# Kernel tuning notes

Measured on AMD Instinct MI355X. Metric: run time of the kernel, lower is better.

The kernel has to match this reference:

```python
import jax, jax.numpy as jnp
import numpy as np

B, N, DIM = 4, 8192, 1024
HEADS, DIM_HEAD = 16, 64


def setup_inputs() -> dict:
    key = jax.random.key(0)
    ks = jax.random.split(key, 6)
    s = 1.0 / np.sqrt(DIM_HEAD)
    so = 1.0 / np.sqrt(HEADS * DIM_HEAD)
    return {
        "x": jax.random.normal(ks[0], (B, N, DIM), dtype=jnp.float32),
        "Wq": jax.random.uniform(ks[1], (DIM_HEAD, DIM_HEAD), jnp.float32, -s, s),
        "Wk": jax.random.uniform(ks[2], (DIM_HEAD, DIM_HEAD), jnp.float32, -s, s),
        "Wv": jax.random.uniform(ks[3], (DIM_HEAD, DIM_HEAD), jnp.float32, -s, s),
        "Wo": jax.random.uniform(ks[4], (DIM, HEADS * DIM_HEAD), jnp.float32, -so, so),
        "bo": jax.random.uniform(ks[5], (DIM,), jnp.float32, -so, so),
    }


def reference(x, Wq, Wk, Wv, Wo, bo):
    Bs, Ns, Cs = x.shape
    # [B, H, N, Dh]
    xh = x.reshape(Bs, Ns, HEADS, DIM_HEAD).transpose(0, 2, 1, 3)
    # torch Linear: y = x @ W.T
    q = jnp.einsum('bhnd,ed->bhne', xh, Wq)
    k = jnp.einsum('bhnd,ed->bhne', xh, Wk)
    v = jnp.einsum('bhnd,ed->bhne', xh, Wv)
    # k^T v: [B, H, Dh, Dh], normalized by N (dropout is identity, p=0)
    dots = jnp.einsum('bhnd,bhne->bhde', k, v) / float(Ns)
    res = jnp.einsum('bhnd,bhde->bhne', q, dots)
    # b h n d -> b n (h d)
    res = res.transpose(0, 2, 1, 3).reshape(Bs, Ns, HEADS * DIM_HEAD)
    return res @ Wo.T + bo
```

## Files before the change

kernel.cpp:

```cpp
#include <hip/hip_runtime.h>

#define DIMC 1024
#define NSEQ 8192
#define DH 64

typedef __attribute__((ext_vector_type(8))) short short8;
typedef __attribute__((ext_vector_type(4))) float f32x4;

__device__ __forceinline__ short f2bf(float f) {
  union { float f; unsigned u; } v; v.f = f;
  unsigned r = v.u + 0x7FFFu + ((v.u >> 16) & 1u);
  return (short)(r >> 16);
}

__device__ __forceinline__ unsigned pack_bf2(float a, float b) {
  union { float f; unsigned u; } va, vb;
  va.f = a; vb.f = b;
  unsigned ua = va.u + 0x8000u;
  unsigned ub = vb.u + 0x8000u;
  return (ua >> 16) | (ub & 0xFFFF0000u);
}

__device__ __forceinline__ unsigned bfbits(float f) {
  union { float f; unsigned u; } v; v.f = f;
  return (v.u + 0x8000u) >> 16;
}
__device__ __forceinline__ float bf2f(unsigned hb) {
  union { unsigned u; float f; } v; v.u = hb << 16;
  return v.f;
}

__device__ __forceinline__ void gload_lds16(const void* g, void* l) {
  __builtin_amdgcn_global_load_lds(
      (const __attribute__((address_space(1))) void*)g,
      (__attribute__((address_space(3))) void*)l, 16, 0, 0);
}

__global__ __launch_bounds__(256) void gram2_kernel(const float* __restrict__ x,
                                                    float* __restrict__ Gpart,
                                                    short* __restrict__ xbf) {
  int chunk = blockIdx.x, bh = blockIdx.y;
  int b = bh >> 4, h = bh & 15;
  int t = threadIdx.x;
  int w = t >> 6, l = t & 63;
  int quad = l >> 4, ln = l & 15;

  __shared__ __align__(16) short XT[4][2][64 * 32];
  short* XH = &XT[w][0][0];
  short* XL = &XT[w][1][0];

  size_t rowbase = (size_t)b * NSEQ + (size_t)chunk * 1024 + w * 256;
  const float* xb = x + rowbase * DIMC + h * DH;
  short* xo = xbf + rowbase * DIMC + h * DH;

  f32x4 acc[4][4];
#pragma unroll
  for (int i = 0; i < 4; i++)
#pragma unroll
    for (int j = 0; j < 4; j++) acc[i][j] = (f32x4){0.f, 0.f, 0.f, 0.f};

  int woff[4][4];
#pragma unroll
  for (int q = 0; q < 4; q++) {
    int kk = 8 * q + 2 * quad;
    int kp = kk ^ ((ln & 3) << 3);
#pragma unroll
    for (int i = 0; i < 4; i++) {
      int d = ln * 4 + i;
      woff[q][i] = d * 32 + kp;
    }
  }
  int roff[4];
  {
    int k0 = (quad * 8) ^ ((ln >> 2) << 3);
#pragma unroll
    for (int i = 0; i < 4; i++) roff[i] = (i * 16 + ln) * 32 + k0;
  }

  float4 cur[4][2];
#pragma unroll
  for (int q = 0; q < 4; q++)
#pragma unroll
    for (int r = 0; r < 2; r++)
      cur[q][r] = *(const float4*)(xb + (size_t)(8 * q + 2 * quad + r) * DIMC + ln * 4);

  for (int ks = 0; ks < 8; ks++) {
    float4 nxt[4][2];
    if (ks < 7) {
      int nb = (ks + 1) * 32;
#pragma unroll
      for (int q = 0; q < 4; q++)
#pragma unroll
        for (int r = 0; r < 2; r++)
          nxt[q][r] = *(const float4*)(xb + (size_t)(nb + 8 * q + 2 * quad + r) * DIMC + ln * 4);
    }
#pragma unroll
    for (int q = 0; q < 4; q++) {
      unsigned h0[4], h1[4], l0[4], l1[4];
#pragma unroll
      for (int i = 0; i < 4; i++) {
        float a = cur[q][0][i], bb = cur[q][1][i];
        h0[i] = bfbits(a); l0[i] = bfbits(a - bf2f(h0[i]));
        h1[i] = bfbits(bb); l1[i] = bfbits(bb - bf2f(h1[i]));
      }
      int grow = ks * 32 + 8 * q + 2 * quad;
      uint2 p0 = {h0[0] | (h0[1] << 16), h0[2] | (h0[3] << 16)};
      uint2 p1 = {h1[0] | (h1[1] << 16), h1[2] | (h1[3] << 16)};
      *(uint2*)(xo + (size_t)grow * DIMC + ln * 4) = p0;
      *(uint2*)(xo + (size_t)(grow + 1) * DIMC + ln * 4) = p1;
#pragma unroll
      for (int i = 0; i < 4; i++) {
        *(unsigned*)&XH[woff[q][i]] = h0[i] | (h1[i] << 16);
        *(unsigned*)&XL[woff[q][i]] = l0[i] | (l1[i] << 16);
      }
    }
    short8 hf[4], lf[4];
#pragma unroll
    for (int i = 0; i < 4; i++) {
      hf[i] = *(const short8*)&XH[roff[i]];
      lf[i] = *(const short8*)&XL[roff[i]];
    }
#pragma unroll
    for (int i = 0; i < 4; i++)
#pragma unroll
      for (int j = 0; j < 4; j++) {
        acc[i][j] = __builtin_amdgcn_mfma_f32_16x16x32_bf16(hf[i], hf[j], acc[i][j], 0, 0, 0);
        acc[i][j] = __builtin_amdgcn_mfma_f32_16x16x32_bf16(hf[i], lf[j], acc[i][j], 0, 0, 0);
        acc[i][j] = __builtin_amdgcn_mfma_f32_16x16x32_bf16(lf[i], hf[j], acc[i][j], 0, 0, 0);
      }
#pragma unroll
    for (int q = 0; q < 4; q++)
#pragma unroll
      for (int r = 0; r < 2; r++) cur[q][r] = nxt[q][r];
  }

  float* gp = Gpart + (size_t)(chunk * 4 + w) * (64 * 4096) + (size_t)bh * 4096;
#pragma unroll
  for (int i = 0; i < 4; i++)
#pragma unroll
    for (int j = 0; j < 4; j++)
#pragma unroll
      for (int r = 0; r < 4; r++) {
        int d = i * 16 + quad * 4 + r, e = j * 16 + ln;
        gp[d * 64 + e] = acc[i][j][r];
      }
}

__global__ __launch_bounds__(64) void gram_kernel(const float* __restrict__ x,
                                                  float* __restrict__ Gpart,
                                                  short* __restrict__ xbf) {
  int chunk = blockIdx.x, bh = blockIdx.y;
  int b = bh >> 4, h = bh & 15;
  int t = threadIdx.x;
  __shared__ __align__(16) float rows[16 * 64];
  const float* xb = x + ((size_t)b * NSEQ) * DIMC + h * DH;
  short* xo = xbf ? xbf + ((size_t)b * NSEQ) * DIMC + h * DH : (short*)0;
  int d0 = (t >> 3) * 8, e0 = (t & 7) * 8;
  float acc[8][8] = {};
  float4 v[4];
#pragma unroll
  for (int i = 0; i < 4; i++) {
    int f4 = i * 64 + t;
    v[i] = *(const float4*)(xb + (size_t)(chunk * 256 + (f4 >> 4)) * DIMC + (f4 & 15) * 4);
  }
  for (int it = 0; it < 16; it++) {
    __syncthreads();
#pragma unroll
    for (int i = 0; i < 4; i++) ((float4*)rows)[i * 64 + t] = v[i];
    __syncthreads();
    if (xo) {
#pragma unroll
      for (int i = 0; i < 4; i++) {
        int f4 = i * 64 + t;
        int row = chunk * 256 + it * 16 + (f4 >> 4), col = (f4 & 15) * 4;
        uint2 pw = {pack_bf2(v[i].x, v[i].y), pack_bf2(v[i].z, v[i].w)};
        *(uint2*)(xo + (size_t)row * DIMC + col) = pw;
      }
    }
    if (it < 15) {
      int nbase = chunk * 256 + (it + 1) * 16;
#pragma unroll
      for (int i = 0; i < 4; i++) {
        int f4 = i * 64 + t;
        v[i] = *(const float4*)(xb + (size_t)(nbase + (f4 >> 4)) * DIMC + (f4 & 15) * 4);
      }
    }
#pragma unroll
    for (int r = 0; r < 16; r++) {
      float xd[8], xe[8];
      *(float4*)&xd[0] = *(const float4*)&rows[r * 64 + d0];
      *(float4*)&xd[4] = *(const float4*)&rows[r * 64 + d0 + 4];
      *(float4*)&xe[0] = *(const float4*)&rows[r * 64 + e0];
      *(float4*)&xe[4] = *(const float4*)&rows[r * 64 + e0 + 4];
#pragma unroll
      for (int i = 0; i < 8; i++)
#pragma unroll
        for (int j = 0; j < 8; j++) acc[i][j] = fmaf(xd[i], xe[j], acc[i][j]);
    }
  }
  float* gp = Gpart + (size_t)chunk * (64 * 4096) + (size_t)bh * 4096;
#pragma unroll
  for (int i = 0; i < 8; i++)
#pragma unroll
    for (int j = 0; j < 8; j++) gp[(d0 + i) * 64 + e0 + j] = acc[i][j];
}

__global__ void reduce_g(const float* __restrict__ Gpart, float* __restrict__ G) {
  int i = blockIdx.x * 256 + threadIdx.x;
  float s = 0.f;
#pragma unroll
  for (int p = 0; p < 32; p++) s += Gpart[(size_t)p * (64 * 4096) + i];
  G[i] = s;
}

__global__ __launch_bounds__(256) void combine_kernel(
    const float* __restrict__ G, const float* __restrict__ Wq,
    const float* __restrict__ Wk, const float* __restrict__ Wv,
    const float* __restrict__ Wo, short* __restrict__ WbigT) {
  int bh = blockIdx.x, qt = blockIdx.y;
  int b = bh >> 4, h = bh & 15;
  int t = threadIdx.x;
  __shared__ __align__(16) float sG[4096];
  __shared__ __align__(16) float sW[4096];
  __shared__ __align__(16) float sA[4096];
  __shared__ __align__(16) float sM[4096];

  for (int i = t; i < 4096; i += 256) sG[i] = G[(size_t)bh * 4096 + i];
  for (int i = t; i < 4096; i += 256) sW[i] = Wk[i];
  __syncthreads();

  int d0 = (t >> 4) * 4, e0 = (t & 15) * 4;
  {
    float a[4][4] = {};
    for (int fg = 0; fg < 16; fg++) {
      float wk[4][4], g4[4][4];
#pragma unroll
      for (int i = 0; i < 4; i++) *(float4*)wk[i] = *(const float4*)&sW[(d0 + i) * 64 + fg * 4];
#pragma unroll
      for (int ff = 0; ff < 4; ff++) *(float4*)g4[ff] = *(const float4*)&sG[(fg * 4 + ff) * 64 + e0];
#pragma unroll
      for (int i = 0; i < 4; i++)
#pragma unroll
        for (int ff = 0; ff < 4; ff++)
#pragma unroll
          for (int j = 0; j < 4; j++) a[i][j] = fmaf(wk[i][ff], g4[ff][j], a[i][j]);
    }
#pragma unroll
    for (int i = 0; i < 4; i++)
#pragma unroll
      for (int j = 0; j < 4; j++) sA[(d0 + i) * 64 + e0 + j] = a[i][j];
  }
  __syncthreads();
  for (int i = t; i < 4096; i += 256) sW[i] = Wv[i];
  __syncthreads();
  {
    float a[4][4] = {};
    for (int fgi = 0; fgi < 16; fgi++) {
      int fg = (fgi + (t & 15)) & 15;
      float t1[4][4], wv[4][4];
#pragma unroll
      for (int i = 0; i < 4; i++) *(float4*)t1[i] = *(const float4*)&sA[(d0 + i) * 64 + fg * 4];
#pragma unroll
      for (int j = 0; j < 4; j++) *(float4*)wv[j] = *(const float4*)&sW[(e0 + j) * 64 + fg * 4];
#pragma unroll
      for (int i = 0; i < 4; i++)
#pragma unroll
        for (int j = 0; j < 4; j++)
#pragma unroll
          for (int ff = 0; ff < 4; ff++) a[i][j] = fmaf(t1[i][ff], wv[j][ff], a[i][j]);
    }
    __syncthreads();
#pragma unroll
    for (int i = 0; i < 4; i++)
#pragma unroll
      for (int j = 0; j < 4; j++) sG[(d0 + i) * 64 + e0 + j] = a[i][j];
  }
  __syncthreads();
  for (int i = t; i < 4096; i += 256) sW[i] = Wq[i];
  __syncthreads();
  {
    float a[4][4] = {};
    for (int f = 0; f < 64; f++) {
      float wq[4], t2[4];
      *(float4*)wq = *(const float4*)&sW[f * 64 + d0];
      *(float4*)t2 = *(const float4*)&sG[f * 64 + e0];
#pragma unroll
      for (int i = 0; i < 4; i++)
#pragma unroll
        for (int j = 0; j < 4; j++) a[i][j] = fmaf(wq[i], t2[j], a[i][j]);
    }
#pragma unroll
    for (int i = 0; i < 4; i++)
#pragma unroll
      for (int j = 0; j < 4; j++) sM[(d0 + i) * 64 + e0 + j] = a[i][j] * (1.0f / 8192.0f);
  }
  __syncthreads();
  int dd0 = (t & 15) * 4, cl0 = (t >> 4) * 4;
  for (int cc = qt * 2; cc < qt * 2 + 2; cc++) {
    int c0 = cc * 64;
    for (int i = t; i < 4096; i += 256)
      sW[i] = Wo[(size_t)(c0 + (i >> 6)) * DIMC + h * DH + (i & 63)];
    __syncthreads();
    float a[4][4] = {};
    for (int egi = 0; egi < 16; egi++) {
      int eg = (egi + (t & 15)) & 15;
      float m4[4][4], wo4[4][4];
#pragma unroll
      for (int i = 0; i < 4; i++) *(float4*)m4[i] = *(const float4*)&sM[(dd0 + i) * 64 + eg * 4];
#pragma unroll
      for (int j = 0; j < 4; j++) *(float4*)wo4[j] = *(const float4*)&sW[(cl0 + j) * 64 + eg * 4];
#pragma unroll
      for (int i = 0; i < 4; i++)
#pragma unroll
        for (int j = 0; j < 4; j++)
#pragma unroll
          for (int ff = 0; ff < 4; ff++) a[i][j] = fmaf(m4[i][ff], wo4[j][ff], a[i][j]);
    }
#pragma unroll
    for (int j = 0; j < 4; j++) {
      uint2 pw = {pack_bf2(a[0][j], a[1][j]), pack_bf2(a[2][j], a[3][j])};
      *(uint2*)&WbigT[((size_t)b << 20) + (size_t)(c0 + cl0 + j) * DIMC + h * DH + dd0] = pw;
    }
    __syncthreads();
  }
}

__global__ __launch_bounds__(256, 3) void gemm_small(
    const float* __restrict__ x, const short* __restrict__ WbigT,
    const float* __restrict__ bo, float* __restrict__ out) {
  int bid = blockIdx.x;
  int xcd = bid & 7, r = bid >> 3;
  int g = r >> 5, q = r & 31;
  int m_blk = g * 32 + xcd * 4 + (q >> 3);
  int n_blk = q & 7;
  int b = m_blk >> 6;
  int row0 = m_blk * 128;
  int c0 = n_blk * 128;

  __shared__ __align__(16) short As[128 * 32];
  __shared__ __align__(16) short Bs[128 * 32];

  int t = threadIdx.x;
  int lane = t & 63, wave = t >> 6;
  int wm = wave >> 1, wn = wave & 1;
  int quad = lane >> 4, ln = lane & 15;

  f32x4 acc[4][4];
#pragma unroll
  for (int i = 0; i < 4; i++)
#pragma unroll
    for (int j = 0; j < 4; j++) acc[i][j] = (f32x4){0.f, 0.f, 0.f, 0.f};

  const short* Bbase = WbigT + ((size_t)b << 20);

  int e_base[2], crow_[2], lc_[2];
#pragma unroll
  for (int L = 0; L < 2; L++) {
    int e = (wave * 2 + L) * 512 + lane * 8;
    e_base[L] = e;
    int crow = e >> 5;
    crow_[L] = crow;
    lc_[L] = ((e >> 3) & 3) ^ ((crow >> 1) & 3);
  }

  for (int kt = 0; kt < 32; kt++) {
    int k0 = kt * 32;
    __syncthreads();
#pragma unroll
    for (int L = 0; L < 2; L++)
      gload_lds16(Bbase + (size_t)(c0 + crow_[L]) * DIMC + k0 + lc_[L] * 8, &Bs[e_base[L]]);
#pragma unroll
    for (int qq = 0; qq < 2; qq++) {
      int elem = qq * 2048 + wave * 512 + lane * 8;
      int m = elem >> 5, kk = elem & 31;
      const float* gp = x + (size_t)(row0 + m) * DIMC + k0 + kk;
      float4 v0 = *(const float4*)gp;
      float4 v1 = *(const float4*)(gp + 4);
      unsigned w0 = pack_bf2(v0.x, v0.y), w1 = pack_bf2(v0.z, v0.w);
      unsigned w2 = pack_bf2(v1.x, v1.y), w3 = pack_bf2(v1.z, v1.w);
      unsigned tmp[4] = {w0, w1, w2, w3};
      int pe = ((elem >> 3) & 3) ^ ((m >> 1) & 3);
      *(short8*)&As[m * 32 + pe * 8] = *(short8*)tmp;
    }
    __syncthreads();
    short8 afrag[4], bfrag[4];
#pragma unroll
    for (int i = 0; i < 4; i++) {
      int ar = wm * 64 + i * 16 + ln;
      afrag[i] = *(const short8*)&As[ar * 32 + (quad ^ ((ar >> 1) & 3)) * 8];
      int br = wn * 64 + i * 16 + ln;
      bfrag[i] = *(const short8*)&Bs[br * 32 + (quad ^ ((br >> 1) & 3)) * 8];
    }
#pragma unroll
    for (int i = 0; i < 4; i++)
#pragma unroll
      for (int j = 0; j < 4; j++)
        acc[i][j] = __builtin_amdgcn_mfma_f32_16x16x32_bf16(afrag[i], bfrag[j], acc[i][j], 0, 0, 0);
  }

  float bov[4];
#pragma unroll
  for (int j = 0; j < 4; j++) bov[j] = bo[c0 + wn * 64 + j * 16 + ln];
#pragma unroll
  for (int i = 0; i < 4; i++)
#pragma unroll
    for (int j = 0; j < 4; j++) {
      int col = c0 + wn * 64 + j * 16 + ln;
#pragma unroll
      for (int rr = 0; rr < 4; rr++) {
        int row = row0 + wm * 64 + i * 16 + quad * 4 + rr;
        out[(size_t)row * DIMC + col] = acc[i][j][rr] + bov[j];
      }
    }
}

__global__ __launch_bounds__(256, 3) void gemm_big(
    const short* __restrict__ xbf, const short* __restrict__ WbigT,
    const float* __restrict__ bo, float* __restrict__ out) {
  int bid = blockIdx.x;
  int xcd = bid & 7, r = bid >> 3;
  int g = r >> 5, q = r & 31;
  int m_blk = g * 32 + xcd * 4 + (q >> 3);
  int n_blk = q & 7;
  int b = m_blk >> 6;
  int row0 = m_blk * 128;
  int c0 = n_blk * 128;

  __shared__ __align__(16) short As[128 * 32];
  __shared__ __align__(16) short Bs[128 * 32];

  int t = threadIdx.x;
  int lane = t & 63, wave = t >> 6;
  int wm = wave >> 1, wn = wave & 1;
  int quad = lane >> 4, ln = lane & 15;

  f32x4 acc[4][4];
#pragma unroll
  for (int i = 0; i < 4; i++)
#pragma unroll
    for (int j = 0; j < 4; j++) acc[i][j] = (f32x4){0.f, 0.f, 0.f, 0.f};

  const short* Bbase = WbigT + ((size_t)b << 20);

  int e_base[2];
  const short* Asrc[2];
  const short* Bsrc[2];
#pragma unroll
  for (int L = 0; L < 2; L++) {
    int e = (wave * 2 + L) * 512 + lane * 8;
    e_base[L] = e;
    int row = e >> 5;
    int lc = ((e >> 3) & 3) ^ ((row >> 1) & 3);
    Asrc[L] = xbf + (size_t)(row0 + row) * DIMC + lc * 8;
    Bsrc[L] = Bbase + (size_t)(c0 + row) * DIMC + lc * 8;
  }

  for (int kt = 0; kt < 32; kt++) {
    int k0 = kt * 32;
    __syncthreads();
#pragma unroll
    for (int L = 0; L < 2; L++) gload_lds16(Asrc[L] + k0, &As[e_base[L]]);
#pragma unroll
    for (int L = 0; L < 2; L++) gload_lds16(Bsrc[L] + k0, &Bs[e_base[L]]);
    __syncthreads();
    short8 afrag[4], bfrag[4];
#pragma unroll
    for (int i = 0; i < 4; i++) {
      int ar = wm * 64 + i * 16 + ln;
      afrag[i] = *(const short8*)&As[ar * 32 + (quad ^ ((ar >> 1) & 3)) * 8];
      int br = wn * 64 + i * 16 + ln;
      bfrag[i] = *(const short8*)&Bs[br * 32 + (quad ^ ((br >> 1) & 3)) * 8];
    }
#pragma unroll
    for (int i = 0; i < 4; i++)
#pragma unroll
      for (int j = 0; j < 4; j++)
        acc[i][j] = __builtin_amdgcn_mfma_f32_16x16x32_bf16(afrag[i], bfrag[j], acc[i][j], 0, 0, 0);
  }

  float bov[4];
#pragma unroll
  for (int j = 0; j < 4; j++) bov[j] = bo[c0 + wn * 64 + j * 16 + ln];
#pragma unroll
  for (int i = 0; i < 4; i++)
#pragma unroll
    for (int j = 0; j < 4; j++) {
      int col = c0 + wn * 64 + j * 16 + ln;
#pragma unroll
      for (int rr = 0; rr < 4; rr++) {
        int row = row0 + wm * 64 + i * 16 + quad * 4 + rr;
        out[(size_t)row * DIMC + col] = acc[i][j][rr] + bov[j];
      }
    }
}

extern "C" void kernel_launch(void* const* d_in, const int* in_sizes, int n_in,
                              void* d_out, int out_size, void* d_ws, size_t ws_size,
                              hipStream_t stream) {
  const float* x  = (const float*)d_in[0];
  const float* Wq = (const float*)d_in[1];
  const float* Wk = (const float*)d_in[2];
  const float* Wv = (const float*)d_in[3];
  const float* Wo = (const float*)d_in[4];
  const float* bo = (const float*)d_in[5];
  float* out = (float*)d_out;
  (void)in_sizes; (void)n_in; (void)out_size;

  if (ws_size >= ((size_t)105 << 20)) {
    short* xbf   = (short*)d_ws;
    float* Gpart = (float*)((char*)d_ws + ((size_t)64 << 20));
    float* G     = (float*)((char*)d_ws + ((size_t)96 << 20));
    short* WbigT = (short*)((char*)d_ws + ((size_t)97 << 20));
    gram2_kernel<<<dim3(8, 64), 256, 0, stream>>>(x, Gpart, xbf);
    reduce_g<<<1024, 256, 0, stream>>>(Gpart, G);
    combine_kernel<<<dim3(64, 8), 256, 0, stream>>>(G, Wq, Wk, Wv, Wo, WbigT);
    gemm_big<<<2048, 256, 0, stream>>>(xbf, WbigT, bo, out);
  } else {
    float* Gpart = (float*)d_ws;
    float* G     = (float*)((char*)d_ws + ((size_t)32 << 20));
    short* WbigT = (short*)((char*)d_ws + ((size_t)33 << 20));
    gram_kernel<<<dim3(32, 64), 64, 0, stream>>>(x, Gpart, (short*)0);
    reduce_g<<<1024, 256, 0, stream>>>(Gpart, G);
    combine_kernel<<<dim3(64, 8), 256, 0, stream>>>(G, Wq, Wk, Wv, Wo, WbigT);
    gemm_small<<<2048, 256, 0, stream>>>(x, WbigT, bo, out);
  }
}
```

Baseline: 375.4 us.

## Rewrite final GEMM with 256x256 tiles, double-buffered LDS and interleaved prefetch

The bf16 output GEMM now uses 512-thread blocks, each computing a 256x256 tile with BK=64. LDS is double-buffered and the next K-slice's global-to-LDS loads are spread across four MFMA phases, with explicit waitcnt, barriers and setprio. The goal is to hide global load latency and raise arithmetic intensity per LDS byte compared with the old 128x128 single-buffered loop. In exchange it uses 128KB of LDS per block and a large accumulator footprint, which limits occupancy, and the grid shrinks to 512 blocks.

```diff
diff --git a/kernel.cpp b/kernel.cpp
--- a/kernel.cpp
+++ b/kernel.cpp
@@ -414,82 +414,162 @@
     }
 }
 
-__global__ __launch_bounds__(256, 3) void gemm_big(
+__global__ __launch_bounds__(512, 2) void gemm_big4(
     const short* __restrict__ xbf, const short* __restrict__ WbigT,
     const float* __restrict__ bo, float* __restrict__ out) {
   int bid = blockIdx.x;
   int xcd = bid & 7, r = bid >> 3;
-  int g = r >> 5, q = r & 31;
-  int m_blk = g * 32 + xcd * 4 + (q >> 3);
-  int n_blk = q & 7;
-  int b = m_blk >> 6;
-  int row0 = m_blk * 128;
-  int c0 = n_blk * 128;
-
-  __shared__ __align__(16) short As[128 * 32];
-  __shared__ __align__(16) short Bs[128 * 32];
+  int m_blk = xcd * 16 + (r >> 2);
+  int n_blk = r & 3;
+  int b = m_blk >> 5;
+  size_t row0 = (size_t)m_blk * 256;
+  int c0 = n_blk * 256;
+
+  __shared__ __align__(16) short As[2][256 * 64];
+  __shared__ __align__(16) short Bs[2][256 * 64];
 
   int t = threadIdx.x;
   int lane = t & 63, wave = t >> 6;
-  int wm = wave >> 1, wn = wave & 1;
+  int wm = wave >> 2, wn = wave & 3;
   int quad = lane >> 4, ln = lane & 15;
 
-  f32x4 acc[4][4];
-#pragma unroll
-  for (int i = 0; i < 4; i++)
+  f32x4 acc[8][4];
+#pragma unroll
+  for (int i = 0; i < 8; i++)
 #pragma unroll
     for (int j = 0; j < 4; j++) acc[i][j] = (f32x4){0.f, 0.f, 0.f, 0.f};
 
   const short* Bbase = WbigT + ((size_t)b << 20);
 
-  int e_base[2];
-  const short* Asrc[2];
-  const short* Bsrc[2];
-#pragma unroll
-  for (int L = 0; L < 2; L++) {
-    int e = (wave * 2 + L) * 512 + lane * 8;
-    e_base[L] = e;
-    int row = e >> 5;
-    int lc = ((e >> 3) & 3) ^ ((row >> 1) & 3);
-    Asrc[L] = xbf + (size_t)(row0 + row) * DIMC + lc * 8;
-    Bsrc[L] = Bbase + (size_t)(c0 + row) * DIMC + lc * 8;
-  }
-
-  for (int kt = 0; kt < 32; kt++) {
-    int k0 = kt * 32;
-    __syncthreads();
-#pragma unroll
-    for (int L = 0; L < 2; L++) gload_lds16(Asrc[L] + k0, &As[e_base[L]]);
-#pragma unroll
-    for (int L = 0; L < 2; L++) gload_lds16(Bsrc[L] + k0, &Bs[e_base[L]]);
-    __syncthreads();
-    short8 afrag[4], bfrag[4];
-#pragma unroll
-    for (int i = 0; i < 4; i++) {
-      int ar = wm * 64 + i * 16 + ln;
-      afrag[i] = *(const short8*)&As[ar * 32 + (quad ^ ((ar >> 1) & 3)) * 8];
-      int br = wn * 64 + i * 16 + ln;
-      bfrag[i] = *(const short8*)&Bs[br * 32 + (quad ^ ((br >> 1) & 3)) * 8];
-    }
-#pragma unroll
-    for (int i = 0; i < 4; i++)
-#pragma unroll
-      for (int j = 0; j < 4; j++)
-        acc[i][j] = __builtin_amdgcn_mfma_f32_16x16x32_bf16(afrag[i], bfrag[j], acc[i][j], 0, 0, 0);
-  }
+  const short* Asrc[4];
+  const short* Bsrc[4];
+  int doff[4];
+#pragma unroll
+  for (int s = 0; s < 4; s++) {
+    int p = s * 512 + t;
+    int row = p >> 3;
+    int cl = (p & 7) ^ (row & 7);
+    doff[s] = p * 8;
+    Asrc[s] = xbf + (row0 + row) * (size_t)DIMC + cl * 8;
+    Bsrc[s] = Bbase + (size_t)(c0 + row) * DIMC + cl * 8;
+  }
+
+#pragma unroll
+  for (int s = 0; s < 4; s++) gload_lds16(Asrc[s], &As[0][doff[s]]);
+#pragma unroll
+  for (int s = 0; s < 4; s++) gload_lds16(Bsrc[s], &Bs[0][doff[s]]);
+
+#define LD_A(dst, i, kk)                                                      \
+  {                                                                           \
+    int ar = wm * 128 + (i)*16 + ln;                                          \
+    dst = *(const short8*)&Ab[ar * 64 + ((((kk)*4 + quad) ^ (ar & 7)) << 3)]; \
+  }
+#define LD_B(dst, j, kk)                                                      \
+  {                                                                           \
+    int br = wn * 64 + (j)*16 + ln;                                           \
+    dst = *(const short8*)&Bb[br * 64 + ((((kk)*4 + quad) ^ (br & 7)) << 3)]; \
+  }
+
+  for (int kt = 0; kt < 16; kt++) {
+    const short* Ab = As[kt & 1];
+    const short* Bb = Bs[kt & 1];
+    short* An = (short*)As[(kt & 1) ^ 1];
+    short* Bn = (short*)Bs[(kt & 1) ^ 1];
+    int kn = (kt + 1) * 64;
+
+    short8 af0[4][2], af1[4][2], bf0[2][2], bf1[2][2], bf0b[2][2];
+
+    if (kt < 15) {
+      gload_lds16(Asrc[0] + kn, &An[doff[0]]);
+      gload_lds16(Asrc[1] + kn, &An[doff[1]]);
+      gload_lds16(Bsrc[0] + kn, &Bn[doff[0]]);
+      gload_lds16(Bsrc[1] + kn, &Bn[doff[1]]);
+      asm volatile("s_waitcnt vmcnt(4)" ::: "memory");
+    } else {
+      asm volatile("s_waitcnt vmcnt(0)" ::: "memory");
+    }
+    __builtin_amdgcn_s_barrier();
+    __builtin_amdgcn_sched_barrier(0);
+#pragma unroll
+    for (int i = 0; i < 4; i++) { LD_A(af0[i][0], i, 0); LD_A(af0[i][1], i, 1); }
+#pragma unroll
+    for (int j = 0; j < 2; j++) { LD_B(bf0[j][0], j, 0); LD_B(bf0[j][1], j, 1); }
+    __builtin_amdgcn_s_setprio(1);
+#pragma unroll
+    for (int i = 0; i < 4; i++)
+#pragma unroll
+      for (int j = 0; j < 2; j++)
+#pragma unroll
+        for (int kk = 0; kk < 2; kk++)
+          acc[i][j] = __builtin_amdgcn_mfma_f32_16x16x32_bf16(af0[i][kk], bf0[j][kk], acc[i][j], 0, 0, 0);
+    __builtin_amdgcn_s_setprio(0);
+    __builtin_amdgcn_s_barrier();
+
+#pragma unroll
+    for (int j = 0; j < 2; j++) { LD_B(bf1[j][0], j + 2, 0); LD_B(bf1[j][1], j + 2, 1); }
+    if (kt < 15) {
+      gload_lds16(Asrc[2] + kn, &An[doff[2]]);
+      gload_lds16(Asrc[3] + kn, &An[doff[3]]);
+    }
+    __builtin_amdgcn_s_barrier();
+    __builtin_amdgcn_s_setprio(1);
+#pragma unroll
+    for (int i = 0; i < 4; i++)
+#pragma unroll
+      for (int j = 0; j < 2; j++)
+#pragma unroll
+        for (int kk = 0; kk < 2; kk++)
+          acc[i][j + 2] = __builtin_amdgcn_mfma_f32_16x16x32_bf16(af0[i][kk], bf1[j][kk], acc[i][j + 2], 0, 0, 0);
+    __builtin_amdgcn_s_setprio(0);
+    __builtin_amdgcn_s_barrier();
+
+#pragma unroll
+    for (int i = 0; i < 4; i++) { LD_A(af1[i][0], i + 4, 0); LD_A(af1[i][1], i + 4, 1); }
+    if (kt < 15) {
+      gload_lds16(Bsrc[2] + kn, &Bn[doff[2]]);
+      gload_lds16(Bsrc[3] + kn, &Bn[doff[3]]);
+    }
+    __builtin_amdgcn_s_barrier();
+    __builtin_amdgcn_s_setprio(1);
+#pragma unroll
+    for (int i = 0; i < 4; i++)
+#pragma unroll
+      for (int j = 0; j < 2; j++)
+#pragma unroll
+        for (int kk = 0; kk < 2; kk++)
+          acc[i + 4][j + 2] = __builtin_amdgcn_mfma_f32_16x16x32_bf16(af1[i][kk], bf1[j][kk], acc[i + 4][j + 2], 0, 0, 0);
+    __builtin_amdgcn_s_setprio(0);
+    __builtin_amdgcn_s_barrier();
+
+#pragma unroll
+    for (int j = 0; j < 2; j++) { LD_B(bf0b[j][0], j, 0); LD_B(bf0b[j][1], j, 1); }
+    __builtin_amdgcn_s_barrier();
+    __builtin_amdgcn_s_setprio(1);
+#pragma unroll
+    for (int i = 0; i < 4; i++)
+#pragma unroll
+      for (int j = 0; j < 2; j++)
+#pragma unroll
+        for (int kk = 0; kk < 2; kk++)
+          acc[i + 4][j] = __builtin_amdgcn_mfma_f32_16x16x32_bf16(af1[i][kk], bf0b[j][kk], acc[i + 4][j], 0, 0, 0);
+    __builtin_amdgcn_s_setprio(0);
+    __builtin_amdgcn_s_barrier();
+  }
+#undef LD_A
+#undef LD_B
 
   float bov[4];
 #pragma unroll
   for (int j = 0; j < 4; j++) bov[j] = bo[c0 + wn * 64 + j * 16 + ln];
 #pragma unroll
-  for (int i = 0; i < 4; i++)
+  for (int i = 0; i < 8; i++)
 #pragma unroll
     for (int j = 0; j < 4; j++) {
       int col = c0 + wn * 64 + j * 16 + ln;
 #pragma unroll
       for (int rr = 0; rr < 4; rr++) {
-        int row = row0 + wm * 64 + i * 16 + quad * 4 + rr;
-        out[(size_t)row * DIMC + col] = acc[i][j][rr] + bov[j];
+        size_t row = row0 + wm * 128 + i * 16 + quad * 4 + rr;
+        out[row * DIMC + col] = acc[i][j][rr] + bov[j];
       }
     }
 }
@@ -514,7 +594,7 @@
     gram2_kernel<<<dim3(8, 64), 256, 0, stream>>>(x, Gpart, xbf);
     reduce_g<<<1024, 256, 0, stream>>>(Gpart, G);
     combine_kernel<<<dim3(64, 8), 256, 0, stream>>>(G, Wq, Wk, Wv, Wo, WbigT);
-    gemm_big<<<2048, 256, 0, stream>>>(xbf, WbigT, bo, out);
+    gemm_big4<<<512, 512, 0, stream>>>(xbf, WbigT, bo, out);
   } else {
     float* Gpart = (float*)d_ws;
     float* G     = (float*)((char*)d_ws + ((size_t)32 << 20));
```

After: 380.8 us. No clear change (+1.4%).
